# Kernel optimization log

Measured on AMD Instinct MI355X. Metric: run time of the kernel, lower is better.

Reference implementation:

```python
import jax, jax.numpy as jnp
import numpy as np

CLASS_DIM = 4   # hardcoded in DsFunction1
PROTO_DIM = 20  # hardcoded in DsFunction1


def setup_inputs() -> dict:
    key = jax.random.key(0)
    k1, k2, k3 = jax.random.split(key, 3)
    B, C, H, Wd, D = 2, 16, 64, 64, 64
    inp = jax.random.normal(k1, (B, C, H, Wd, D), dtype=jnp.float32)
    W = jax.random.normal(k2, (PROTO_DIM, C), dtype=jnp.float32)
    BETA = jax.random.normal(k3, (PROTO_DIM, CLASS_DIM), dtype=jnp.float32) * 0.5
    alpha = jnp.zeros((PROTO_DIM, 1), dtype=jnp.float32)           # init 0 per reset_parameters
    gamma = jnp.full((PROTO_DIM, 1), 0.1, dtype=jnp.float32)       # init 0.1 per reset_parameters
    return {"input": inp, "W": W, "BETA": BETA, "alpha": alpha, "gamma": gamma}


def _ds_forward(x, W, BETA, alpha, gamma):
    # x: [B,C,H,Wd,D]; W: [K,C]; BETA: [K,M]; alpha, gamma: [K,1]
    B, C, H, Wd, D = x.shape
    BETA2 = BETA * BETA
    U = BETA2 / jnp.sum(BETA2, axis=1, keepdims=True)              # [K,M] membership weights
    alphap = 0.99 / (1.0 + jnp.exp(-alpha[:, 0]))                  # [K]

    # squared distances to prototypes: d[k] = 0.5 * ||x - W_k||^2 over channel dim
    x2 = jnp.sum(x * x, axis=1)                                    # [B,H,Wd,D]
    xw = jnp.einsum('bchwd,kc->kbhwd', x, W)                       # [K,B,H,Wd,D]
    w2 = jnp.sum(W * W, axis=1)                                    # [K]
    d = 0.5 * (x2[None] - 2.0 * xw + w2[:, None, None, None, None])  # [K,B,H,Wd,D]

    g2 = (gamma[:, 0] ** 2)[:, None, None, None, None]
    s = alphap[:, None, None, None, None] * jnp.exp(-g2 * d)       # [K,B,H,Wd,D]

    mfoc = U[:, :, None, None, None, None] * s[:, None]            # [K,M,B,H,Wd,D] focal masses
    momega = 1.0 - s                                               # [K,B,H,Wd,D] mass on Omega

    # sequential Dempster (unnormalized conjunctive) combination over prototypes
    def step(carry, km):
        mk_f, mk_o = carry                                         # [M,B,H,Wd,D], [B,H,Wd,D]
        m_f, m_o = km
        new_f = mk_f * (m_f + m_o[None]) + m_f * mk_o[None]
        new_o = mk_o * m_o
        return (new_f, new_o), None

    init = (jnp.zeros((CLASS_DIM, B, H, Wd, D), x.dtype),
            jnp.ones((B, H, Wd, D), x.dtype))
    (mk_f, mk_o), _ = jax.lax.scan(step, init, (mfoc, momega))

    mk = jnp.concatenate([mk_f, mk_o[None]], axis=0)               # [M+1,B,H,Wd,D]
    mk_n = mk / jnp.sum(mk, axis=0, keepdims=True)                 # normalize masses
    return jnp.transpose(mk_n, (1, 0, 2, 3, 4))                    # [B,M+1,H,Wd,D]


def reference(input, W, BETA, alpha, gamma):
    return _ds_forward(input, W, BETA, alpha, gamma)
```

## Files before the change

### kernel.cpp

```cpp
#include <hip/hip_runtime.h>
#include <hip/hip_bf16.h>
#include <math.h>

#define NK 20
#define NC 16
#define NM 4
#define TSTEP 2

typedef __attribute__((ext_vector_type(8)))  short  short8;
typedef __attribute__((ext_vector_type(16))) float  floatx16;

static __device__ __forceinline__ short bf16b(float f) {
    __hip_bfloat16 h = __float2bfloat16(f);
    return *reinterpret_cast<short*>(&h);
}

__global__ __launch_bounds__(256, 4) void ds_fused(
    const float* __restrict__ inp,
    const float* __restrict__ Wg,
    const float* __restrict__ BETAg,
    const float* __restrict__ alphag,
    const float* __restrict__ gammag,
    float* __restrict__ out,
    int S,
    int BS)
{
    __shared__ __align__(16) float sCst[32][8];
    __shared__ __align__(16) short sWpb[32][16];
    __shared__ short sA2[32][2];

    const int t = threadIdx.x;
    if (t < 32) {
        if (t < NK) {
            const float L   = 1.4426950408889634f;
            const float g   = gammag[t];
            const float g2L = g * g * L;
            float w2 = 0.f;
            #pragma unroll
            for (int c = 0; c < NC; ++c) {
                const float w = Wg[t*NC + c];
                sWpb[t][c] = bf16b(g2L * w);
                w2 = fmaf(w, w, w2);
            }
            const float a = 0.99f / (1.0f + __expf(-alphag[t]));
            float b0 = BETAg[t*NM+0], b1 = BETAg[t*NM+1], b2 = BETAg[t*NM+2], b3 = BETAg[t*NM+3];
            b0 *= b0; b1 *= b1; b2 *= b2; b3 *= b3;
            const float uinv = 1.0f / (b0 + b1 + b2 + b3);
            sCst[t][0] = (1.0f - b0*uinv) * a;
            sCst[t][1] = (1.0f - b1*uinv) * a;
            sCst[t][2] = (1.0f - b2*uinv) * a;
            sCst[t][3] = (1.0f - b3*uinv) * a;
            sCst[t][4] = a;
            sCst[t][5] = 0.f; sCst[t][6] = 0.f; sCst[t][7] = 0.f;
            sA2[t][0] = bf16b(-0.5f * g2L);
            sA2[t][1] = bf16b(-0.5f * g2L * w2);
        } else {
            #pragma unroll
            for (int i = 0; i < 8; ++i) sCst[t][i] = 0.f;
            #pragma unroll
            for (int c = 0; c < NC; ++c) sWpb[t][c] = 0;
            sA2[t][0] = 0; sA2[t][1] = 0;
        }
    }
    __syncthreads();

    const int lane = t & 63;
    const int half = lane >> 5;
    const int col  = lane & 31;
    const int gw   = blockIdx.x * 4 + (t >> 6);
    const int ebase = gw * (TSTEP * 32);

    const int b  = (ebase >= S) ? 1 : 0;
    const int spw = ebase - b * S;
    const float* xb0 = inp + (size_t)b * NC * S + spw + col;
    float xv[TSTEP][8];
    #pragma unroll
    for (int tt = 0; tt < TSTEP; ++tt)
        #pragma unroll
        for (int j = 0; j < 8; ++j)
            xv[tt][j] = xb0[(size_t)(8*half + j) * S + tt*32];

    const short8 afrag = *(const short8*)&sWpb[col][half*8];
    short8 a2frag;
    #pragma unroll
    for (int j = 0; j < 8; ++j) a2frag[j] = 0;
    if (half == 0) { a2frag[0] = sA2[col][0]; a2frag[1] = sA2[col][1]; }

    float cm0[12], cm1[12], cm2[12], cm3[12], cO[12];
    #pragma unroll
    for (int r = 0; r < 12; ++r) {
        const int p = (r & 3) + 8*(r >> 2) + 4*half;
        const float4 cv = *(const float4*)&sCst[p][0];
        cm0[r] = cv.x; cm1[r] = cv.y; cm2[r] = cv.z; cm3[r] = cv.w;
        cO[r]  = sCst[p][4];
    }

    #pragma unroll
    for (int tt = 0; tt < TSTEP; ++tt) {
        const int sp = spw + tt*32 + col;

        short8 bfrag;
        float x2p = 0.f;
        #pragma unroll
        for (int j = 0; j < 8; ++j) {
            const float v = xv[tt][j];
            x2p = fmaf(v, v, x2p);
            bfrag[j] = bf16b(v);
        }
        const float x2 = x2p + __shfl_xor(x2p, 32, 64);

        short8 b2frag;
        #pragma unroll
        for (int j = 0; j < 8; ++j) b2frag[j] = 0;
        if (half == 0) { b2frag[0] = bf16b(x2); b2frag[1] = (short)0x3F80; }

        floatx16 acc;
        #pragma unroll
        for (int i = 0; i < 16; ++i) acc[i] = 0.f;
        acc = __builtin_amdgcn_mfma_f32_32x32x16_bf16(afrag,  bfrag,  acc, 0, 0, 0);
        acc = __builtin_amdgcn_mfma_f32_32x32x16_bf16(a2frag, b2frag, acc, 0, 0, 0);

        float P0 = 1.f, P1 = 1.f, P2 = 1.f, P3 = 1.f, PO = 1.f;
        #pragma unroll
        for (int r = 0; r < 12; ++r) {
            const float ek = __builtin_amdgcn_exp2f(acc[r]);
            P0 *= fmaf(-cm0[r], ek, 1.0f);
            P1 *= fmaf(-cm1[r], ek, 1.0f);
            P2 *= fmaf(-cm2[r], ek, 1.0f);
            P3 *= fmaf(-cm3[r], ek, 1.0f);
            PO *= fmaf(-cO[r],  ek, 1.0f);
        }
        P0 *= __shfl_xor(P0, 32, 64);
        P1 *= __shfl_xor(P1, 32, 64);
        P2 *= __shfl_xor(P2, 32, 64);
        P3 *= __shfl_xor(P3, 32, 64);
        PO *= __shfl_xor(PO, 32, 64);

        const float O  = PO;
        const float f0 = P0 - O, f1 = P1 - O, f2 = P2 - O, f3 = P3 - O;
        const float inv = 1.0f / (f0 + f1 + f2 + f3 + O);

        float* op = out + (size_t)b * (NM+1) * S + sp;
        if (half == 0) {
            op[0]           = f0 * inv;
            op[(size_t)S]   = f1 * inv;
            op[(size_t)2*S] = f2 * inv;
        } else {
            op[(size_t)3*S] = f3 * inv;
            op[(size_t)4*S] = O  * inv;
        }
    }
}

extern "C" void kernel_launch(void* const* d_in, const int* in_sizes, int n_in,
                              void* d_out, int out_size, void* d_ws, size_t ws_size,
                              hipStream_t stream) {
    const float* inp   = (const float*)d_in[0];
    const float* Wg    = (const float*)d_in[1];
    const float* BETAg = (const float*)d_in[2];
    const float* alphag= (const float*)d_in[3];
    const float* gammag= (const float*)d_in[4];
    float* out = (float*)d_out;

    const int BS = in_sizes[0] / NC;
    const int S  = BS / 2;

    const int elems_per_block = 4 * TSTEP * 32;
    const int grid = (BS + elems_per_block - 1) / elems_per_block;
    ds_fused<<<grid, 256, 0, stream>>>(inp, Wg, BETAg, alphag, gammag, out, S, BS);
}
```

Measured before the change: 85.20 us.

## Pack prototypes into 10 rows per half, fold w2 into constants, compute x² via MFMA

```diff
diff --git a/kernel.cpp b/kernel.cpp
--- a/kernel.cpp
+++ b/kernel.cpp
@@ -27,40 +27,44 @@
 {
     __shared__ __align__(16) float sCst[32][8];
     __shared__ __align__(16) short sWpb[32][16];
-    __shared__ short sA2[32][2];
+    __shared__ short sNh[32];
 
     const int t = threadIdx.x;
+
     if (t < 32) {
-        if (t < NK) {
-            const float L   = 1.4426950408889634f;
-            const float g   = gammag[t];
-            const float g2L = g * g * L;
-            float w2 = 0.f;
-            #pragma unroll
-            for (int c = 0; c < NC; ++c) {
-                const float w = Wg[t*NC + c];
-                sWpb[t][c] = bf16b(g2L * w);
-                w2 = fmaf(w, w, w2);
-            }
-            const float a = 0.99f / (1.0f + __expf(-alphag[t]));
-            float b0 = BETAg[t*NM+0], b1 = BETAg[t*NM+1], b2 = BETAg[t*NM+2], b3 = BETAg[t*NM+3];
-            b0 *= b0; b1 *= b1; b2 *= b2; b3 *= b3;
-            const float uinv = 1.0f / (b0 + b1 + b2 + b3);
-            sCst[t][0] = (1.0f - b0*uinv) * a;
-            sCst[t][1] = (1.0f - b1*uinv) * a;
-            sCst[t][2] = (1.0f - b2*uinv) * a;
-            sCst[t][3] = (1.0f - b3*uinv) * a;
-            sCst[t][4] = a;
-            sCst[t][5] = 0.f; sCst[t][6] = 0.f; sCst[t][7] = 0.f;
-            sA2[t][0] = bf16b(-0.5f * g2L);
-            sA2[t][1] = bf16b(-0.5f * g2L * w2);
-        } else {
-            #pragma unroll
-            for (int i = 0; i < 8; ++i) sCst[t][i] = 0.f;
-            #pragma unroll
-            for (int c = 0; c < NC; ++c) sWpb[t][c] = 0;
-            sA2[t][0] = 0; sA2[t][1] = 0;
+        #pragma unroll
+        for (int i = 0; i < 8; ++i) sCst[t][i] = 0.f;
+        #pragma unroll
+        for (int c = 0; c < NC; ++c) sWpb[t][c] = 0;
+        sNh[t] = 0;
+    }
+    __syncthreads();
+    if (t < NK) {
+        const float L   = 1.4426950408889634f;
+        const float g   = gammag[t];
+        const float g2L = g * g * L;
+        const int tm  = (t < 10) ? t : (t - 10);
+        const int row = (tm & 3) + 8 * (tm >> 2) + ((t < 10) ? 0 : 4);
+        float w2 = 0.f;
+        #pragma unroll
+        for (int c = 0; c < NC; ++c) {
+            const float w = Wg[t*NC + c];
+            sWpb[row][c] = bf16b(g2L * w);
+            w2 = fmaf(w, w, w2);
         }
+        const float nh = -0.5f * g2L;
+        sNh[row] = bf16b(nh);
+        const float p2nbk = exp2f(nh * w2);
+        const float a  = 0.99f / (1.0f + __expf(-alphag[t]));
+        const float ap = a * p2nbk;
+        float b0 = BETAg[t*NM+0], b1 = BETAg[t*NM+1], b2 = BETAg[t*NM+2], b3 = BETAg[t*NM+3];
+        b0 *= b0; b1 *= b1; b2 *= b2; b3 *= b3;
+        const float uinv = 1.0f / (b0 + b1 + b2 + b3);
+        sCst[row][0] = (1.0f - b0*uinv) * ap;
+        sCst[row][1] = (1.0f - b1*uinv) * ap;
+        sCst[row][2] = (1.0f - b2*uinv) * ap;
+        sCst[row][3] = (1.0f - b3*uinv) * ap;
+        sCst[row][4] = ap;
     }
     __syncthreads();
 
@@ -70,7 +74,7 @@
     const int gw   = blockIdx.x * 4 + (t >> 6);
     const int ebase = gw * (TSTEP * 32);
 
-    const int b  = (ebase >= S) ? 1 : 0;
+    const int b   = (ebase >= S) ? 1 : 0;
     const int spw = ebase - b * S;
     const float* xb0 = inp + (size_t)b * NC * S + spw + col;
     float xv[TSTEP][8];
@@ -81,54 +85,41 @@
             xv[tt][j] = xb0[(size_t)(8*half + j) * S + tt*32];
 
     const short8 afrag = *(const short8*)&sWpb[col][half*8];
-    short8 a2frag;
+    const short  nhb   = sNh[col];
+    short8 nhfrag;
     #pragma unroll
-    for (int j = 0; j < 8; ++j) a2frag[j] = 0;
-    if (half == 0) { a2frag[0] = sA2[col][0]; a2frag[1] = sA2[col][1]; }
-
-    float cm0[12], cm1[12], cm2[12], cm3[12], cO[12];
-    #pragma unroll
-    for (int r = 0; r < 12; ++r) {
-        const int p = (r & 3) + 8*(r >> 2) + 4*half;
-        const float4 cv = *(const float4*)&sCst[p][0];
-        cm0[r] = cv.x; cm1[r] = cv.y; cm2[r] = cv.z; cm3[r] = cv.w;
-        cO[r]  = sCst[p][4];
-    }
+    for (int j = 0; j < 8; ++j) nhfrag[j] = nhb;
 
     #pragma unroll
     for (int tt = 0; tt < TSTEP; ++tt) {
         const int sp = spw + tt*32 + col;
 
-        short8 bfrag;
-        float x2p = 0.f;
+        short8 bfrag, b2frag;
         #pragma unroll
         for (int j = 0; j < 8; ++j) {
             const float v = xv[tt][j];
-            x2p = fmaf(v, v, x2p);
-            bfrag[j] = bf16b(v);
+            bfrag[j]  = bf16b(v);
+            b2frag[j] = bf16b(v * v);
         }
-        const float x2 = x2p + __shfl_xor(x2p, 32, 64);
-
-        short8 b2frag;
-        #pragma unroll
-        for (int j = 0; j < 8; ++j) b2frag[j] = 0;
-        if (half == 0) { b2frag[0] = bf16b(x2); b2frag[1] = (short)0x3F80; }
 
         floatx16 acc;
         #pragma unroll
         for (int i = 0; i < 16; ++i) acc[i] = 0.f;
         acc = __builtin_amdgcn_mfma_f32_32x32x16_bf16(afrag,  bfrag,  acc, 0, 0, 0);
-        acc = __builtin_amdgcn_mfma_f32_32x32x16_bf16(a2frag, b2frag, acc, 0, 0, 0);
+        acc = __builtin_amdgcn_mfma_f32_32x32x16_bf16(nhfrag, b2frag, acc, 0, 0, 0);
 
         float P0 = 1.f, P1 = 1.f, P2 = 1.f, P3 = 1.f, PO = 1.f;
         #pragma unroll
-        for (int r = 0; r < 12; ++r) {
-            const float ek = __builtin_amdgcn_exp2f(acc[r]);
-            P0 *= fmaf(-cm0[r], ek, 1.0f);
-            P1 *= fmaf(-cm1[r], ek, 1.0f);
-            P2 *= fmaf(-cm2[r], ek, 1.0f);
-            P3 *= fmaf(-cm3[r], ek, 1.0f);
-            PO *= fmaf(-cO[r],  ek, 1.0f);
+        for (int r = 0; r < 10; ++r) {
+            const int p = (r & 3) + 8*(r >> 2) + 4*half;
+            const float4 cv = *(const float4*)&sCst[p][0];
+            const float  aO = sCst[p][4];
+            const float  ek = __builtin_amdgcn_exp2f(acc[r]);
+            P0 *= fmaf(-cv.x, ek, 1.0f);
+            P1 *= fmaf(-cv.y, ek, 1.0f);
+            P2 *= fmaf(-cv.z, ek, 1.0f);
+            P3 *= fmaf(-cv.w, ek, 1.0f);
+            PO *= fmaf(-aO,   ek, 1.0f);
         }
         P0 *= __shfl_xor(P0, 32, 64);
         P1 *= __shfl_xor(P1, 32, 64);
```

Result: no change. 84.05 us (-1.3%).
